# Kernel optimization log

Hardware: AMD Instinct MI355X
Metric: run time of the kernel (lower is better)

The kernel has to match this reference:

```python
import jax, jax.numpy as jnp
import numpy as np

N_NODES = 50000
N_EDGES = 1200000
IN_CH = 128
HID = 64
HEADS = 1
OUT_CH = 64
NEG_SLOPE = 0.2


def setup_inputs() -> dict:
    key = jax.random.key(0)
    ks = jax.random.split(key, 9)
    x = jax.random.normal(ks[0], (N_NODES, IN_CH), dtype=jnp.float32)
    edge_index = jax.random.randint(ks[1], (2, N_EDGES), 0, N_NODES, dtype=jnp.int64)
    edge_weight = jax.random.uniform(ks[2], (N_EDGES,), dtype=jnp.float32)
    # GATv2Conv params: separate lin_l / lin_r (share_weights=False), attention vector, bias
    s_in = 1.0 / np.sqrt(IN_CH)
    W_l = jax.random.uniform(ks[3], (HEADS * HID, IN_CH), minval=-s_in, maxval=s_in, dtype=jnp.float32)
    W_r = jax.random.uniform(ks[4], (HEADS * HID, IN_CH), minval=-s_in, maxval=s_in, dtype=jnp.float32)
    att = jax.random.normal(ks[5], (HEADS, HID), dtype=jnp.float32) * (1.0 / np.sqrt(HID))
    bias_conv = jnp.zeros((HEADS * HID,), dtype=jnp.float32)
    s_h = 1.0 / np.sqrt(HEADS * HID)
    W_lin = jax.random.uniform(ks[6], (OUT_CH, HEADS * HID), minval=-s_h, maxval=s_h, dtype=jnp.float32)
    b_lin = jax.random.uniform(ks[7], (OUT_CH,), minval=-s_h, maxval=s_h, dtype=jnp.float32)
    return {"x": x, "edge_index": edge_index, "edge_weight": edge_weight,
            "W_l": W_l, "W_r": W_r, "att": att, "bias_conv": bias_conv,
            "W_lin": W_lin, "b_lin": b_lin}


def reference(x, edge_index, edge_weight, W_l, W_r, att, bias_conv, W_lin, b_lin):
    N = x.shape[0]
    H, C = att.shape
    # add self loops (GATv2Conv default add_self_loops=True)
    loop = jnp.arange(N, dtype=edge_index.dtype)
    src = jnp.concatenate([edge_index[0], loop])  # [E+N] source j
    dst = jnp.concatenate([edge_index[1], loop])  # [E+N] target i
    # linear projections -> [N, H, C]
    xl = (x @ W_l.T).reshape(N, H, C)
    xr = (x @ W_r.T).reshape(N, H, C)
    # per-edge GATv2 logits: att . LeakyReLU(xl_j + xr_i)
    e = jax.nn.leaky_relu(xl[src] + xr[dst], NEG_SLOPE)       # [E, H, C]
    logits = jnp.einsum('ehc,hc->eh', e, att)                 # [E, H]
    # segment softmax over incoming edges of each target node
    m = jax.ops.segment_max(logits, dst, num_segments=N)       # [N, H]
    m = jnp.where(jnp.isfinite(m), m, 0.0)
    expv = jnp.exp(logits - m[dst])                            # [E, H]
    denom = jax.ops.segment_sum(expv, dst, num_segments=N)     # [N, H]
    alpha = expv / (denom[dst] + 1e-16)                        # [E, H]
    # dropout(p=0.2) on alpha: identity in eval mode
    # scatter-weighted aggregation of source features
    msg = alpha[:, :, None] * xl[src]                          # [E, H, C]
    out = jax.ops.segment_sum(msg, dst, num_segments=N)        # [N, H, C]
    out = out.reshape(N, H * C) + bias_conv
    out = jax.nn.elu(out)
    return out @ W_lin.T + b_lin
```

## Files before the change

kernel.cpp:

```cpp
#include <hip/hip_runtime.h>

#define IN_CH 128
#define HID 64
#define NEG 0.2f

typedef short bf16x8 __attribute__((ext_vector_type(8)));
typedef float f32x4  __attribute__((ext_vector_type(4)));

__device__ __forceinline__ unsigned short f2bf(float f) {
    unsigned u = __float_as_uint(f);
    u += 0x7fffu + ((u >> 16) & 1u);
    return (unsigned short)(u >> 16);
}
__device__ __forceinline__ float bf2f(unsigned short h) {
    return __uint_as_float((unsigned)h << 16);
}

__global__ __launch_bounds__(512, 4) void proj_part(
    const float* __restrict__ x, const float* __restrict__ W_l,
    const float* __restrict__ W_r,
    unsigned short* __restrict__ xlb, float* __restrict__ xr,
    const int* __restrict__ src, const int* __restrict__ dst,
    int* __restrict__ gcursor, unsigned* __restrict__ pairs,
    int nN, int E)
{
    __shared__ unsigned short A_hi[64 * 136];
    __shared__ unsigned short A_lo[64 * 136];
    int tid = threadIdx.x;
    int nb = blockIdx.x * 64;
    int lane = tid & 63;
    int wid = __builtin_amdgcn_readfirstlane(tid >> 6);
    int mat = wid >> 2;
    int ct  = (wid & 3) * 16;
    int n = lane & 15, quad = lane >> 4;

    const float* __restrict__ W = mat ? W_r : W_l;
    bf16x8 Bh[4], Bl[4];
    #pragma unroll
    for (int s = 0; s < 4; ++s) {
        const float* wr = W + (size_t)(ct + n) * IN_CH + s * 32 + quad * 8;
        float4 w0 = *(const float4*)(wr);
        float4 w1 = *(const float4*)(wr + 4);
        float wf[8] = {w0.x, w0.y, w0.z, w0.w, w1.x, w1.y, w1.z, w1.w};
        #pragma unroll
        for (int j = 0; j < 8; ++j) {
            unsigned short h = f2bf(wf[j]);
            Bh[s][j] = (short)h;
            Bl[s][j] = (short)f2bf(wf[j] - bf2f(h));
        }
    }

    #pragma unroll
    for (int it = 0; it < 2; ++it) {
        int gi = it * 512 + tid;
        int row = gi >> 4, c8 = gi & 15;
        int node = nb + row;
        uint4 hi = make_uint4(0, 0, 0, 0), lo = make_uint4(0, 0, 0, 0);
        if (node < nN) {
            const float* xp = x + (size_t)node * IN_CH + c8 * 8;
            float4 f0 = *(const float4*)(xp);
            float4 f1 = *(const float4*)(xp + 4);
            float xf[8] = {f0.x, f0.y, f0.z, f0.w, f1.x, f1.y, f1.z, f1.w};
            unsigned hh[8], ll[8];
            #pragma unroll
            for (int j = 0; j < 8; ++j) {
                unsigned short h = f2bf(xf[j]);
                hh[j] = h;
                ll[j] = f2bf(xf[j] - bf2f(h));
            }
            hi = make_uint4(hh[0] | (hh[1] << 16), hh[2] | (hh[3] << 16),
                            hh[4] | (hh[5] << 16), hh[6] | (hh[7] << 16));
            lo = make_uint4(ll[0] | (ll[1] << 16), ll[2] | (ll[3] << 16),
                            ll[4] | (ll[5] << 16), ll[6] | (ll[7] << 16));
        }
        *(uint4*)(&A_hi[row * 136 + c8 * 8]) = hi;
        *(uint4*)(&A_lo[row * 136 + c8 * 8]) = lo;
    }
    __syncthreads();

    #pragma unroll
    for (int mt = 0; mt < 4; ++mt) {
        f32x4 d = {0.f, 0.f, 0.f, 0.f};
        int arow = (mt * 16 + n) * 136 + quad * 8;
        #pragma unroll
        for (int s = 0; s < 4; ++s) {
            bf16x8 ah = *(const bf16x8*)(&A_hi[arow + s * 32]);
            bf16x8 al = *(const bf16x8*)(&A_lo[arow + s * 32]);
            d = __builtin_amdgcn_mfma_f32_16x16x32_bf16(ah, Bh[s], d, 0, 0, 0);
            d = __builtin_amdgcn_mfma_f32_16x16x32_bf16(ah, Bl[s], d, 0, 0, 0);
            d = __builtin_amdgcn_mfma_f32_16x16x32_bf16(al, Bh[s], d, 0, 0, 0);
        }
        #pragma unroll
        for (int r = 0; r < 4; ++r) {
            int node = nb + mt * 16 + quad * 4 + r;
            if (node < nN) {
                if (mat)
                    xr[(size_t)node * HID + ct + n] = d[r];
                else
                    xlb[(size_t)node * HID + ct + n] = f2bf(d[r]);
            }
        }
    }

    __syncthreads();
    int PB = ((int)gridDim.x + 3) >> 2;
    if ((int)blockIdx.x < PB) {
        int* lh = (int*)A_hi;
        int* lb = (int*)A_lo;
        for (int i = tid; i < 4096; i += 512) lh[i] = 0;
        __syncthreads();

        int C = ((E + PB - 1) / PB + 3) & ~3;
        int lo = blockIdx.x * C;
        int hi = lo + C; if (hi > E) hi = E;

        unsigned pw[12];
        unsigned rk[12];
        #pragma unroll
        for (int s = 0; s < 3; ++s) {
            int i0 = lo + s * 2048 + tid * 4;
            int4 s4, d4;
            bool full = (i0 + 3 < hi);
            if (full) {
                s4 = *(const int4*)(src + i0);
                d4 = *(const int4*)(dst + i0);
            }
            #pragma unroll
            for (int j = 0; j < 4; ++j) {
                int q = s * 4 + j;
                int e = i0 + j;
                int sv = 0, dv = 0;
                bool ok;
                if (full) {
                    sv = (&s4.x)[j]; dv = (&d4.x)[j]; ok = true;
                } else {
                    ok = (e < hi);
                    if (ok) { sv = src[e]; dv = dst[e]; }
                }
                if (ok) {
                    int b = dv >> 4;
                    pw[q] = (unsigned)sv | (((unsigned)dv & 15u) << 16)
                                         | ((unsigned)b << 20);
                    rk[q] = (unsigned)atomicAdd(&lh[b], 1);
                } else {
                    pw[q] = 0xFFFFFFFFu;
                    rk[q] = 0;
                }
            }
        }
        __syncthreads();
        for (int i = tid; i < 4096; i += 512) {
            int c = lh[i];
            lb[i] = c ? atomicAdd(&gcursor[i], c) : 0;
        }
        __syncthreads();
        #pragma unroll
        for (int q = 0; q < 12; ++q) {
            if (pw[q] != 0xFFFFFFFFu) {
                int b = (int)(pw[q] >> 20);
                int p = lb[b] + (int)rk[q];
                if (p < 512) pairs[(b << 9) + p] = pw[q] & 0xFFFFFu;
            }
        }
    }
}

#define LOADQ(U0, U1, U2, U3, BASE)                                          \
    {                                                                        \
        int kb_ = (BASE) + g * 4;                                            \
        int k0_ = (kb_     <= last) ? kb_     : last;                        \
        int k1_ = (kb_ + 1 <= last) ? kb_ + 1 : last;                        \
        int k2_ = (kb_ + 2 <= last) ? kb_ + 2 : last;                        \
        int k3_ = (kb_ + 3 <= last) ? kb_ + 3 : last;                        \
        int j0_ = sorted[k0_], j1_ = sorted[k1_];                            \
        int j2_ = sorted[k2_], j3_ = sorted[k3_];                            \
        U0 = *(const ushort4*)(xlb + (size_t)j0_ * HID + gl * 4);            \
        U1 = *(const ushort4*)(xlb + (size_t)j1_ * HID + gl * 4);            \
        U2 = *(const ushort4*)(xlb + (size_t)j2_ * HID + gl * 4);            \
        U3 = *(const ushort4*)(xlb + (size_t)j3_ * HID + gl * 4);            \
    }

#define COMPQ(U0, U1, U2, U3, BASE)                                          \
    {                                                                        \
        int kb_ = (BASE) + g * 4;                                            \
        float xax = bf2f(U0.x), xay = bf2f(U0.y), xaz = bf2f(U0.z), xaw = bf2f(U0.w); \
        float xbx = bf2f(U1.x), xby = bf2f(U1.y), xbz = bf2f(U1.z), xbw = bf2f(U1.w); \
        float xcx = bf2f(U2.x), xcy = bf2f(U2.y), xcz = bf2f(U2.z), xcw = bf2f(U2.w); \
        float xdx = bf2f(U3.x), xdy = bf2f(U3.y), xdz = bf2f(U3.z), xdw = bf2f(U3.w); \
        float t0, t1, t2, t3, ra, rb, rc, rd;                                \
        t0 = xax + xr4.x; t1 = xay + xr4.y; t2 = xaz + xr4.z; t3 = xaw + xr4.w; \
        ra = a1.x * t0;          ra = fmaf(a2.x, fabsf(t0), ra);             \
        ra = fmaf(a1.y, t1, ra); ra = fmaf(a2.y, fabsf(t1), ra);             \
        ra = fmaf(a1.z, t2, ra); ra = fmaf(a2.z, fabsf(t2), ra);             \
        ra = fmaf(a1.w, t3, ra); ra = fmaf(a2.w, fabsf(t3), ra);             \
        t0 = xbx + xr4.x; t1 = xby + xr4.y; t2 = xbz + xr4.z; t3 = xbw + xr4.w; \
        rb = a1.x * t0;          rb = fmaf(a2.x, fabsf(t0), rb);             \
        rb = fmaf(a1.y, t1, rb); rb = fmaf(a2.y, fabsf(t1), rb);             \
        rb = fmaf(a1.z, t2, rb); rb = fmaf(a2.z, fabsf(t2), rb);             \
        rb = fmaf(a1.w, t3, rb); rb = fmaf(a2.w, fabsf(t3), rb);             \
        t0 = xcx + xr4.x; t1 = xcy + xr4.y; t2 = xcz + xr4.z; t3 = xcw + xr4.w; \
        rc = a1.x * t0;          rc = fmaf(a2.x, fabsf(t0), rc);             \
        rc = fmaf(a1.y, t1, rc); rc = fmaf(a2.y, fabsf(t1), rc);             \
        rc = fmaf(a1.z, t2, rc); rc = fmaf(a2.z, fabsf(t2), rc);             \
        rc = fmaf(a1.w, t3, rc); rc = fmaf(a2.w, fabsf(t3), rc);             \
        t0 = xdx + xr4.x; t1 = xdy + xr4.y; t2 = xdz + xr4.z; t3 = xdw + xr4.w; \
        rd = a1.x * t0;          rd = fmaf(a2.x, fabsf(t0), rd);             \
        rd = fmaf(a1.y, t1, rd); rd = fmaf(a2.y, fabsf(t1), rd);             \
        rd = fmaf(a1.z, t2, rd); rd = fmaf(a2.z, fabsf(t2), rd);             \
        rd = fmaf(a1.w, t3, rd); rd = fmaf(a2.w, fabsf(t3), rd);             \
        ra += __shfl_xor(ra, 1, 64); rb += __shfl_xor(rb, 1, 64);            \
        rc += __shfl_xor(rc, 1, 64); rd += __shfl_xor(rd, 1, 64);            \
        ra += __shfl_xor(ra, 2, 64); rb += __shfl_xor(rb, 2, 64);            \
        rc += __shfl_xor(rc, 2, 64); rd += __shfl_xor(rd, 2, 64);            \
        ra += __shfl_xor(ra, 4, 64); rb += __shfl_xor(rb, 4, 64);            \
        rc += __shfl_xor(rc, 4, 64); rd += __shfl_xor(rd, 4, 64);            \
        ra += __shfl_xor(ra, 8, 64); rb += __shfl_xor(rb, 8, 64);            \
        rc += __shfl_xor(rc, 8, 64); rd += __shfl_xor(rd, 8, 64);            \
        float ea = (kb_     < s1) ? __expf(ra) : 0.f;                        \
        float eb = (kb_ + 1 < s1) ? __expf(rb) : 0.f;                        \
        float ec = (kb_ + 2 < s1) ? __expf(rc) : 0.f;                        \
        float ed = (kb_ + 3 < s1) ? __expf(rd) : 0.f;                        \
        denom += (ea + eb) + (ec + ed);                                      \
        acc.x = fmaf(ea, xax, acc.x); acc.x = fmaf(eb, xbx, acc.x);          \
        acc.x = fmaf(ec, xcx, acc.x); acc.x = fmaf(ed, xdx, acc.x);          \
        acc.y = fmaf(ea, xay, acc.y); acc.y = fmaf(eb, xby, acc.y);          \
        acc.y = fmaf(ec, xcy, acc.y); acc.y = fmaf(ed, xdy, acc.y);          \
        acc.z = fmaf(ea, xaz, acc.z); acc.z = fmaf(eb, xbz, acc.z);          \
        acc.z = fmaf(ec, xcz, acc.z); acc.z = fmaf(ed, xdz, acc.z);          \
        acc.w = fmaf(ea, xaw, acc.w); acc.w = fmaf(eb, xbw, acc.w);          \
        acc.w = fmaf(ec, xcw, acc.w); acc.w = fmaf(ed, xdw, acc.w);          \
    }

__global__ __launch_bounds__(256, 8) void gat_sorted(
    const unsigned short* __restrict__ xlb, const float* __restrict__ xr,
    const unsigned* __restrict__ pairs, const int* __restrict__ bcnt,
    const float* __restrict__ att, const float* __restrict__ bias_conv,
    const float* __restrict__ W_lin, const float* __restrict__ b_lin,
    float* __restrict__ out, int nN)
{
    __shared__ unsigned short sorted[512];
    __shared__ unsigned short Hhi[16 * 72];
    __shared__ unsigned short Hlo[16 * 72];
    __shared__ int cnt[16];
    __shared__ int rs[17];
    int tid = threadIdx.x;
    if (tid < 16) cnt[tid] = 0;
    __syncthreads();

    int blk = blockIdx.x;
    int M = bcnt[blk];
    if (M > 512) M = 512;
    const unsigned* __restrict__ pb = pairs + ((size_t)blk << 9);

    unsigned ew[2];
    int dl[2], rk[2];
    int ne = 0;
    for (int i = tid; i < M; i += 256) {
        unsigned w = pb[i];
        ew[ne] = w;
        dl[ne] = (w >> 16) & 15;
        rk[ne] = atomicAdd(&cnt[dl[ne]], 1);
        ++ne;
    }
    __syncthreads();
    if (tid < 16) {
        int c = cnt[tid];
        int s = c;
        #pragma unroll
        for (int d = 1; d < 16; d <<= 1) {
            int t = __shfl_up(s, d, 64);
            if (tid >= d) s += t;
        }
        rs[tid] = s - c;
        if (tid == 15) rs[16] = s;
    }
    __syncthreads();
    for (int q = 0; q < ne; ++q)
        sorted[rs[dl[q]] + rk[q]] = (unsigned short)(ew[q] & 0xFFFFu);
    __syncthreads();

    int lane = tid & 63, wv = tid >> 6;
    int g = lane >> 4, gl = lane & 15;
    const float4 att4 = *(const float4*)(att + gl * 4);
    const float c1 = 0.5f * (1.f + NEG), c2 = 0.5f * (1.f - NEG);
    float4 a1 = make_float4(c1 * att4.x, c1 * att4.y, c1 * att4.z, c1 * att4.w);
    float4 a2 = make_float4(c2 * att4.x, c2 * att4.y, c2 * att4.z, c2 * att4.w);
    int nb = blk * 16;
    for (int t = 0; t < 4; ++t) {
        int nl = wv * 4 + t;
        int node = nb + nl;
        if (node >= nN) break;
        const float4 xr4 = *(const float4*)(xr + (size_t)node * HID + gl * 4);
        float4 acc = make_float4(0.f, 0.f, 0.f, 0.f);
        float denom = 0.f;
        int s0 = rs[nl], s1 = rs[nl + 1];
        int last = s1 - 1;

        ushort4 A0, A1_, A2_, A3;
        ushort4 B0, B1_, B2_, B3;
        if (s0 < s1) LOADQ(A0, A1_, A2_, A3, s0);

        if (g == 0) {
            ushort4 us = *(const ushort4*)(xlb + (size_t)node * HID + gl * 4);
            float xsx = bf2f(us.x), xsy = bf2f(us.y), xsz = bf2f(us.z), xsw = bf2f(us.w);
            float tx = xsx + xr4.x, ty = xsy + xr4.y;
            float tz = xsz + xr4.z, tw = xsw + xr4.w;
            float r = a1.x * tx;
            r = fmaf(a2.x, fabsf(tx), r);
            r = fmaf(a1.y, ty, r); r = fmaf(a2.y, fabsf(ty), r);
            r = fmaf(a1.z, tz, r); r = fmaf(a2.z, fabsf(tz), r);
            r = fmaf(a1.w, tw, r); r = fmaf(a2.w, fabsf(tw), r);
            r += __shfl_xor(r, 1, 64);
            r += __shfl_xor(r, 2, 64);
            r += __shfl_xor(r, 4, 64);
            r += __shfl_xor(r, 8, 64);
            float ev = __expf(r);
            denom = ev;
            acc.x = ev * xsx; acc.y = ev * xsy;
            acc.z = ev * xsz; acc.w = ev * xsw;
        }

        if (s0 < s1) {
            int base = s0;
            while (true) {
                int nx = base + 16;
                if (nx < s1) LOADQ(B0, B1_, B2_, B3, nx);
                COMPQ(A0, A1_, A2_, A3, base);
                base = nx;
                if (base >= s1) break;
                nx = base + 16;
                if (nx < s1) LOADQ(A0, A1_, A2_, A3, nx);
                COMPQ(B0, B1_, B2_, B3, base);
                base = nx;
                if (base >= s1) break;
            }
        }

        denom += __shfl_xor(denom, 16, 64);
        denom += __shfl_xor(denom, 32, 64);
        acc.x += __shfl_xor(acc.x, 16, 64); acc.x += __shfl_xor(acc.x, 32, 64);
        acc.y += __shfl_xor(acc.y, 16, 64); acc.y += __shfl_xor(acc.y, 32, 64);
        acc.z += __shfl_xor(acc.z, 16, 64); acc.z += __shfl_xor(acc.z, 32, 64);
        acc.w += __shfl_xor(acc.w, 16, 64); acc.w += __shfl_xor(acc.w, 32, 64);
        float inv = 1.f / (denom + 1e-16f);
        float4 b4 = *(const float4*)(bias_conv + gl * 4);
        float hx = fmaf(acc.x, inv, b4.x);
        float hy = fmaf(acc.y, inv, b4.y);
        float hz = fmaf(acc.z, inv, b4.z);
        float hw = fmaf(acc.w, inv, b4.w);
        hx = (hx > 0.f) ? hx : (__expf(hx) - 1.f);
        hy = (hy > 0.f) ? hy : (__expf(hy) - 1.f);
        hz = (hz > 0.f) ? hz : (__expf(hz) - 1.f);
        hw = (hw > 0.f) ? hw : (__expf(hw) - 1.f);
        if (g == 0) {
            unsigned short hix = f2bf(hx), hiy = f2bf(hy),
                           hiz = f2bf(hz), hiw = f2bf(hw);
            ushort4 vhi = make_ushort4(hix, hiy, hiz, hiw);
            ushort4 vlo = make_ushort4(f2bf(hx - bf2f(hix)), f2bf(hy - bf2f(hiy)),
                                       f2bf(hz - bf2f(hiz)), f2bf(hw - bf2f(hiw)));
            *(ushort4*)(&Hhi[nl * 72 + gl * 4]) = vhi;
            *(ushort4*)(&Hlo[nl * 72 + gl * 4]) = vlo;
        }
    }
    __syncthreads();

    bf16x8 Wh[2], Wl[2];
    #pragma unroll
    for (int s = 0; s < 2; ++s) {
        const float* wr = W_lin + (size_t)(wv * 16 + gl) * HID + s * 32 + g * 8;
        float4 w0 = *(const float4*)(wr);
        float4 w1 = *(const float4*)(wr + 4);
        float wf[8] = {w0.x, w0.y, w0.z, w0.w, w1.x, w1.y, w1.z, w1.w};
        #pragma unroll
        for (int j = 0; j < 8; ++j) {
            unsigned short h = f2bf(wf[j]);
            Wh[s][j] = (short)h;
            Wl[s][j] = (short)f2bf(wf[j] - bf2f(h));
        }
    }
    float blin = b_lin[wv * 16 + gl];
    {
        f32x4 d = {0.f, 0.f, 0.f, 0.f};
        int arow = gl * 72 + g * 8;
        #pragma unroll
        for (int s = 0; s < 2; ++s) {
            bf16x8 ah = *(const bf16x8*)(&Hhi[arow + s * 32]);
            bf16x8 al = *(const bf16x8*)(&Hlo[arow + s * 32]);
            d = __builtin_amdgcn_mfma_f32_16x16x32_bf16(ah, Wh[s], d, 0, 0, 0);
            d = __builtin_amdgcn_mfma_f32_16x16x32_bf16(ah, Wl[s], d, 0, 0, 0);
            d = __builtin_amdgcn_mfma_f32_16x16x32_bf16(al, Wh[s], d, 0, 0, 0);
        }
        #pragma unroll
        for (int r = 0; r < 4; ++r) {
            int node = nb + g * 4 + r;
            if (node < nN)
                out[(size_t)node * HID + wv * 16 + gl] = d[r] + blin;
        }
    }
}

extern "C" void kernel_launch(void* const* d_in, const int* in_sizes, int n_in,
                              void* d_out, int out_size, void* d_ws, size_t ws_size,
                              hipStream_t stream) {
    const float* x      = (const float*)d_in[0];
    const int*   ei     = (const int*)d_in[1];
    const float* W_l    = (const float*)d_in[3];
    const float* W_r    = (const float*)d_in[4];
    const float* att    = (const float*)d_in[5];
    const float* bias_c = (const float*)d_in[6];
    const float* W_lin  = (const float*)d_in[7];
    const float* b_lin  = (const float*)d_in[8];
    float* out = (float*)d_out;

    int N = in_sizes[0] / IN_CH;
    int E = in_sizes[2];
    const int* srcp = ei;
    const int* dstp = ei + E;
    int NB = (N + 63) / 64;
    int NQ = (N + 15) / 16;

    char* ws = (char*)d_ws;
    float* xr = (float*)ws;
    unsigned short* xlb = (unsigned short*)(xr + (size_t)N * HID);
    int* gcursor = (int*)(xlb + (size_t)N * HID);
    unsigned* pairs = (unsigned*)(gcursor + 4096);

    hipMemsetAsync(gcursor, 0, 4096 * sizeof(int), stream);
    proj_part<<<NB, 512, 0, stream>>>(x, W_l, W_r, xlb, xr, srcp, dstp,
                                      gcursor, pairs, N, E);
    gat_sorted<<<NQ, 256, 0, stream>>>(xlb, xr, pairs, gcursor,
                                       att, bias_c, W_lin, b_lin, out, N);
}
```

Before: 198.1 us.

## Prefetch next node's first edge batch across node loop iterations

Moves the software pipelining from within a node's edge list to across nodes: the first 16-edge batch of the next node is loaded while the current node is processed. Within a node, the remaining batches are now loaded and computed without double buffering. This targets the latency stall at the start of each node, since most nodes have about 24 in-edges (one or two batches). The trade-off is that nodes with many batches lose intra-node overlap, and out-of-range nodes are now clamped instead of breaking out of the loop, so a few redundant loads occur.

```diff
diff --git a/kernel.cpp b/kernel.cpp
--- a/kernel.cpp
+++ b/kernel.cpp
@@ -165,13 +165,13 @@
     }
 }
 
-#define LOADQ(U0, U1, U2, U3, BASE)                                          \
+#define LOADQ(U0, U1, U2, U3, BASE, LASTC)                                   \
     {                                                                        \
         int kb_ = (BASE) + g * 4;                                            \
-        int k0_ = (kb_     <= last) ? kb_     : last;                        \
-        int k1_ = (kb_ + 1 <= last) ? kb_ + 1 : last;                        \
-        int k2_ = (kb_ + 2 <= last) ? kb_ + 2 : last;                        \
-        int k3_ = (kb_ + 3 <= last) ? kb_ + 3 : last;                        \
+        int k0_ = (kb_     <= (LASTC)) ? kb_     : (LASTC);                  \
+        int k1_ = (kb_ + 1 <= (LASTC)) ? kb_ + 1 : (LASTC);                  \
+        int k2_ = (kb_ + 2 <= (LASTC)) ? kb_ + 2 : (LASTC);                  \
+        int k3_ = (kb_ + 3 <= (LASTC)) ? kb_ + 3 : (LASTC);                  \
         int j0_ = sorted[k0_], j1_ = sorted[k1_];                            \
         int j2_ = sorted[k2_], j3_ = sorted[k3_];                            \
         U0 = *(const ushort4*)(xlb + (size_t)j0_ * HID + gl * 4);            \
@@ -286,22 +286,37 @@
     float4 a1 = make_float4(c1 * att4.x, c1 * att4.y, c1 * att4.z, c1 * att4.w);
     float4 a2 = make_float4(c2 * att4.x, c2 * att4.y, c2 * att4.z, c2 * att4.w);
     int nb = blk * 16;
+
+    ushort4 P0, P1, P2, P3;
+    ushort4 A0, A1_, A2_, A3_;
+    {
+        int nl0 = wv * 4;
+        int s0p = rs[nl0], s1p = rs[nl0 + 1];
+        int lastp = (s1p > s0p) ? (s1p - 1) : s0p;
+        if (lastp > 511) lastp = 511;
+        LOADQ(P0, P1, P2, P3, s0p, lastp);
+    }
+
     for (int t = 0; t < 4; ++t) {
         int nl = wv * 4 + t;
         int node = nb + nl;
-        if (node >= nN) break;
-        const float4 xr4 = *(const float4*)(xr + (size_t)node * HID + gl * 4);
+        int nodec = (node < nN) ? node : (nN - 1);
+        const float4 xr4 = *(const float4*)(xr + (size_t)nodec * HID + gl * 4);
+
+        A0 = P0; A1_ = P1; A2_ = P2; A3_ = P3;
+        int s0 = rs[nl], s1 = rs[nl + 1];
+        {
+            int nn2 = (nl + 2 > 16) ? 16 : (nl + 2);
+            int s0n = rs[nl + 1], s1n = rs[nn2];
+            int lastn = (s1n > s0n) ? (s1n - 1) : s0n;
+            if (lastn > 511) lastn = 511;
+            LOADQ(P0, P1, P2, P3, s0n, lastn);
+        }
+
         float4 acc = make_float4(0.f, 0.f, 0.f, 0.f);
         float denom = 0.f;
-        int s0 = rs[nl], s1 = rs[nl + 1];
-        int last = s1 - 1;
-
-        ushort4 A0, A1_, A2_, A3;
-        ushort4 B0, B1_, B2_, B3;
-        if (s0 < s1) LOADQ(A0, A1_, A2_, A3, s0);
-
         if (g == 0) {
-            ushort4 us = *(const ushort4*)(xlb + (size_t)node * HID + gl * 4);
+            ushort4 us = *(const ushort4*)(xlb + (size_t)nodec * HID + gl * 4);
             float xsx = bf2f(us.x), xsy = bf2f(us.y), xsz = bf2f(us.z), xsw = bf2f(us.w);
             float tx = xsx + xr4.x, ty = xsy + xr4.y;
             float tz = xsz + xr4.z, tw = xsw + xr4.w;
@@ -321,18 +336,12 @@
         }
 
         if (s0 < s1) {
-            int base = s0;
-            while (true) {
-                int nx = base + 16;
-                if (nx < s1) LOADQ(B0, B1_, B2_, B3, nx);
-                COMPQ(A0, A1_, A2_, A3, base);
-                base = nx;
-                if (base >= s1) break;
-                nx = base + 16;
-                if (nx < s1) LOADQ(A0, A1_, A2_, A3, nx);
-                COMPQ(B0, B1_, B2_, B3, base);
-                base = nx;
-                if (base >= s1) break;
+            int last = s1 - 1;
+            COMPQ(A0, A1_, A2_, A3_, s0);
+            for (int base = s0 + 16; base < s1; base += 16) {
+                ushort4 U0, U1, U2, U3;
+                LOADQ(U0, U1, U2, U3, base, last);
+                COMPQ(U0, U1, U2, U3, base);
             }
         }
 
```

After: 168.2 us. 1.18x faster.
